# Performance work log

Measured on AMD Instinct MI355X. Metric: run time of the kernel, lower is better.

The kernel has to match this reference:

```python
import jax, jax.numpy as jnp
import numpy as np
import math

B, C, RES, N, H = 32, 32, 16, 16384, 64
G = RES ** 3
RATIO = 1.0


def _halton2(n):
    # 2-D Halton sequence (radical inverse, bases 2 and 3), shape (2, n)
    def radinv(idx, base):
        inv = np.zeros(n, dtype=np.float64)
        f = 1.0 / base
        i = idx.copy()
        while i.max() > 0:
            inv += f * (i % base)
            i //= base
            f /= base
        return inv
    idx = np.arange(1, n + 1)
    return np.stack([radinv(idx, 2), radinv(idx, 3)], axis=0).astype(np.float32)


def setup_inputs() -> dict:
    key = jax.random.key(0)
    ks = jax.random.split(key, 3)
    rng = np.random.default_rng(0)
    x = jax.random.normal(ks[0], (B, C, RES, RES, RES), dtype=jnp.float32)
    # density-driven counts: per-batch multinomial allocation summing exactly to N
    dens = rng.random((B, G)) ** 2
    probs = dens / dens.sum(axis=1, keepdims=True)
    counts = np.stack([rng.multinomial(N, probs[b]) for b in range(B)]).astype(np.int32)
    # grid offsets: ((meshgrid + 0.5) / res - 0.5).view(3, -1)  (normalize_ratio = 0.5)
    grid = np.stack(np.meshgrid(np.arange(RES), np.arange(RES), np.arange(RES), indexing='ij'), 0).astype(np.float32)
    grid_o = ((grid + 0.5) / RES - 0.5).reshape(3, -1)
    # Halton noise scaled: b_rnd * ratio - ratio/2, broadcast to batch
    b_rnd = _halton2(N) * RATIO - RATIO / 2.0
    b_rnd = np.broadcast_to(b_rnd[None], (B, 2, N)).copy()
    # pointwise generator MLP: (C+2) -> H -> 3
    W1 = jax.random.normal(ks[1], (H, C + 2), dtype=jnp.float32) * 0.05
    b1 = jnp.zeros((H,), dtype=jnp.float32)
    W2 = jax.random.normal(ks[2], (3, H), dtype=jnp.float32) * 0.05
    b2 = jnp.zeros((3,), dtype=jnp.float32)
    return {"x": x, "counts": jnp.asarray(counts), "b_rnd": jnp.asarray(b_rnd),
            "grid_o": jnp.asarray(grid_o), "W1": W1, "b1": b1, "W2": W2, "b2": b2}


def reference(x, counts, b_rnd, grid_o, W1, b1, W2, b2):
    b, c = x.shape[0], x.shape[1]
    n = b_rnd.shape[-1]
    xf = x.reshape(b, c, -1)                      # (b, c, G)
    # repeat_interleave(x[:, ind], counts[ind]) with fixed output size n:
    # output slot j maps to cell idx = searchsorted(cumsum(counts), j, 'right')
    cum = jnp.cumsum(counts, axis=1)              # (b, G)
    slots = jnp.arange(n)
    idx = jax.vmap(lambda cs: jnp.searchsorted(cs, slots, side='right'))(cum)  # (b, n)
    x_ind = jnp.take_along_axis(xf, idx[:, None, :], axis=2)                   # (b, c, n)
    o_ind = jnp.transpose(grid_o[:, idx], (1, 0, 2))                           # (b, 3, n)
    b_inp = jnp.concatenate([x_ind, b_rnd], axis=1)                            # (b, c+2, n)
    h = jax.nn.relu(jnp.einsum('hc,bcn->bhn', W1, b_inp) + b1[None, :, None])
    out = jnp.einsum('oh,bhn->bon', W2, h) + b2[None, :, None]                 # (b, 3, n)
    norm = jnp.linalg.norm(out, axis=1)                                        # (b, n)
    reg = jnp.clip(norm - math.sqrt(3.0) / RES, 0.0)
    return out + o_ind, reg
```

## Files before the change

kernel.cpp:

```cpp
#include <hip/hip_runtime.h>
#include <math.h>

constexpr int B_ = 32;
constexpr int C_ = 32;
constexpr int RES_ = 16;
constexpr int G_ = RES_ * RES_ * RES_;
constexpr int N_ = 16384;
constexpr int H_ = 64;
__device__ constexpr float REG_THR = 0.10825317547305483f;

__global__ __launch_bounds__(256) void expand_kernel(const int* __restrict__ counts,
                                                     int* __restrict__ idx_arr) {
    const int b = blockIdx.x;
    const int* cb = counts + b * G_;
    int* ib = idx_arr + b * N_;

    __shared__ int partials[256];
    const int t = threadIdx.x;
    const int base = t * 16;

    int local[16];
    int s = 0;
#pragma unroll
    for (int i = 0; i < 16; ++i) {
        s += cb[base + i];
        local[i] = s;
    }
    partials[t] = s;
    __syncthreads();

    for (int off = 1; off < 256; off <<= 1) {
        int v = (t >= off) ? partials[t - off] : 0;
        __syncthreads();
        partials[t] += v;
        __syncthreads();
    }
    const int prev = (t > 0) ? partials[t - 1] : 0;

#pragma unroll
    for (int i = 0; i < 16; ++i) {
        const int start = prev + (i > 0 ? local[i - 1] : 0);
        const int end   = prev + local[i];
        for (int j = start; j < end; ++j) ib[j] = base + i;
    }
}

__global__ __launch_bounds__(256) void mlp_kernel(
    const float* __restrict__ x, const float* __restrict__ b_rnd,
    const float* __restrict__ grid_o, const float* __restrict__ W1,
    const float* __restrict__ b1, const float* __restrict__ W2,
    const float* __restrict__ b2, const int* __restrict__ idx_arr,
    float* __restrict__ out0, float* __restrict__ reg_out) {
    const int b = blockIdx.y;
    const int n = blockIdx.x * 256 + threadIdx.x;

    const int idx = idx_arr[b * N_ + n];

    float inp[34];
    const float* xb = x + ((size_t)b * C_) * G_ + idx;
#pragma unroll
    for (int c = 0; c < C_; ++c) inp[c] = xb[(size_t)c * G_];
    inp[32] = b_rnd[((size_t)b * 2 + 0) * N_ + n];
    inp[33] = b_rnd[((size_t)b * 2 + 1) * N_ + n];

    float o0 = b2[0], o1 = b2[1], o2 = b2[2];
#pragma unroll 4
    for (int h = 0; h < H_; ++h) {
        float acc = b1[h];
        const float* w = W1 + h * 34;
#pragma unroll
        for (int c = 0; c < 34; ++c) acc = fmaf(w[c], inp[c], acc);
        acc = fmaxf(acc, 0.0f);
        o0 = fmaf(W2[0 * H_ + h], acc, o0);
        o1 = fmaf(W2[1 * H_ + h], acc, o1);
        o2 = fmaf(W2[2 * H_ + h], acc, o2);
    }

    const float nrm = sqrtf(o0 * o0 + o1 * o1 + o2 * o2);
    const float reg = fmaxf(nrm - REG_THR, 0.0f);

    o0 += grid_o[0 * G_ + idx];
    o1 += grid_o[1 * G_ + idx];
    o2 += grid_o[2 * G_ + idx];

    float* p = out0 + ((size_t)b * 3) * N_ + n;
    p[0]              = o0;
    p[N_]             = o1;
    p[2 * (size_t)N_] = o2;
    reg_out[(size_t)b * N_ + n] = reg;
}

extern "C" void kernel_launch(void* const* d_in, const int* in_sizes, int n_in,
                              void* d_out, int out_size, void* d_ws, size_t ws_size,
                              hipStream_t stream) {
    const float* x      = (const float*)d_in[0];
    const int*   counts = (const int*)  d_in[1];
    const float* b_rnd  = (const float*)d_in[2];
    const float* grid_o = (const float*)d_in[3];
    const float* W1     = (const float*)d_in[4];
    const float* b1     = (const float*)d_in[5];
    const float* W2     = (const float*)d_in[6];
    const float* b2     = (const float*)d_in[7];

    float* out  = (float*)d_out;
    float* rout = out + (size_t)B_ * 3 * N_;
    int*   idx_arr = (int*)d_ws;

    expand_kernel<<<B_, 256, 0, stream>>>(counts, idx_arr);

    dim3 grid(N_ / 256, B_);
    mlp_kernel<<<grid, 256, 0, stream>>>(x, b_rnd, grid_o, W1, b1, W2, b2,
                                         idx_arr, out, rout);
}
```

Baseline: 126.2 us.

## Replace serial slot expansion with shared-memory binary search in MLP kernel

The expand kernel no longer writes slot indices with serial per-thread loops. It now writes only the inclusive cumsum. Each MLP block loads that batch's cumsum (4096 ints) into shared memory and binary-searches to find the cell for each slot, which removes the serialized, imbalanced writes in a 32-block kernel. In exchange every block reloads 16KB of cumsum and does 12 LDS lookups, and the shared memory use may reduce occupancy. Empty asm barriers on the inputs also pin them in registers.

```diff
diff --git a/kernel.cpp b/kernel.cpp
--- a/kernel.cpp
+++ b/kernel.cpp
@@ -9,11 +9,11 @@
 constexpr int H_ = 64;
 __device__ constexpr float REG_THR = 0.10825317547305483f;
 
-__global__ __launch_bounds__(256) void expand_kernel(const int* __restrict__ counts,
-                                                     int* __restrict__ idx_arr) {
+__global__ __launch_bounds__(256) void scan_kernel(const int* __restrict__ counts,
+                                                   int* __restrict__ cum) {
     const int b = blockIdx.x;
     const int* cb = counts + b * G_;
-    int* ib = idx_arr + b * N_;
+    int* ob = cum + b * G_;
 
     __shared__ int partials[256];
     const int t = threadIdx.x;
@@ -38,23 +38,33 @@
     const int prev = (t > 0) ? partials[t - 1] : 0;
 
 #pragma unroll
-    for (int i = 0; i < 16; ++i) {
-        const int start = prev + (i > 0 ? local[i - 1] : 0);
-        const int end   = prev + local[i];
-        for (int j = start; j < end; ++j) ib[j] = base + i;
-    }
+    for (int i = 0; i < 16; ++i) ob[base + i] = prev + local[i];
 }
 
 __global__ __launch_bounds__(256) void mlp_kernel(
     const float* __restrict__ x, const float* __restrict__ b_rnd,
     const float* __restrict__ grid_o, const float* __restrict__ W1,
     const float* __restrict__ b1, const float* __restrict__ W2,
-    const float* __restrict__ b2, const int* __restrict__ idx_arr,
+    const float* __restrict__ b2, const int* __restrict__ cum,
     float* __restrict__ out0, float* __restrict__ reg_out) {
     const int b = blockIdx.y;
     const int n = blockIdx.x * 256 + threadIdx.x;
+    const int t = threadIdx.x;
 
-    const int idx = idx_arr[b * N_ + n];
+    __shared__ int s_cum[G_];
+    const int* cb = cum + b * G_;
+#pragma unroll
+    for (int i = 0; i < G_ / 256; ++i) s_cum[t + i * 256] = cb[t + i * 256];
+    __syncthreads();
+
+    int lo = 0, hi = G_ - 1;
+#pragma unroll
+    for (int it = 0; it < 12; ++it) {
+        const int mid = (lo + hi) >> 1;
+        if (s_cum[mid] > n) hi = mid; else lo = mid + 1;
+        if (lo >= hi) { hi = lo; }
+    }
+    const int idx = lo;
 
     float inp[34];
     const float* xb = x + ((size_t)b * C_) * G_ + idx;
@@ -62,6 +72,9 @@
     for (int c = 0; c < C_; ++c) inp[c] = xb[(size_t)c * G_];
     inp[32] = b_rnd[((size_t)b * 2 + 0) * N_ + n];
     inp[33] = b_rnd[((size_t)b * 2 + 1) * N_ + n];
+
+#pragma unroll
+    for (int c = 0; c < 34; ++c) asm volatile("" : "+v"(inp[c]));
 
     float o0 = b2[0], o1 = b2[1], o2 = b2[2];
 #pragma unroll 4
@@ -104,11 +117,11 @@
 
     float* out  = (float*)d_out;
     float* rout = out + (size_t)B_ * 3 * N_;
-    int*   idx_arr = (int*)d_ws;
+    int*   cum  = (int*)d_ws;
 
-    expand_kernel<<<B_, 256, 0, stream>>>(counts, idx_arr);
+    scan_kernel<<<B_, 256, 0, stream>>>(counts, cum);
 
     dim3 grid(N_ / 256, B_);
     mlp_kernel<<<grid, 256, 0, stream>>>(x, b_rnd, grid_o, W1, b1, W2, b2,
-                                         idx_arr, out, rout);
+                                         cum, out, rout);
 }
```

Result: faster. 122.0 us (-3.3%).
